# Kernel optimization log

Hardware: AMD Instinct MI355X
Metric: run time of the kernel (lower is better)

## Reference

```python
import jax, jax.numpy as jnp
import numpy as np

LMAX, MMAX = 4, 2
C_SPH = 32           # sphere_channels
H = 128              # edge hidden channels
N_SPECIES = 90
RESCALE = 5.0
M_SIZE_0 = LMAX + 1                                   # 5
NUM_COEFFS = sum(2 * min(l, MMAX) + 1 for l in range(LMAX + 1))  # 19
K_FULL = (LMAX + 1) ** 2                              # 25
N_NODES = 20000
N_EDGES = 320000
D_EDGE = 128
EPS = 1e-6


def layer_norm(x, scale, bias):
    mu = jnp.mean(x, axis=-1, keepdims=True)
    var = jnp.mean(jnp.square(x - mu), axis=-1, keepdims=True)
    return (x - mu) * jax.lax.rsqrt(var + EPS) * scale + bias


def setup_inputs() -> dict:
    key = jax.random.key(0)
    ks = jax.random.split(key, 12)
    node_species = jax.random.randint(ks[0], (N_NODES,), 0, N_SPECIES)
    edge_embeds = jax.random.normal(ks[1], (N_EDGES, D_EDGE), dtype=jnp.float32)
    senders = jax.random.randint(ks[2], (N_EDGES,), 0, N_NODES)
    receivers = jax.random.randint(ks[3], (N_EDGES,), 0, N_NODES)
    wigner_inv = jax.random.normal(ks[4], (N_EDGES, K_FULL, NUM_COEFFS), dtype=jnp.float32)
    # learned params
    embed_table = jax.random.normal(ks[5], (N_SPECIES, 2 * H), dtype=jnp.float32) * 0.001
    d_in = D_EDGE + 2 * H  # concat(edge, sender_emb, receiver_emb)
    W0 = jax.random.normal(ks[6], (d_in, H), dtype=jnp.float32) / np.sqrt(d_in)
    b0 = jnp.zeros((H,), jnp.float32)
    ln0_s = jnp.ones((H,), jnp.float32); ln0_b = jnp.zeros((H,), jnp.float32)
    W1 = jax.random.normal(ks[7], (H, H), dtype=jnp.float32) / np.sqrt(H)
    b1 = jnp.zeros((H,), jnp.float32)
    ln1_s = jnp.ones((H,), jnp.float32); ln1_b = jnp.zeros((H,), jnp.float32)
    W2 = jax.random.normal(ks[8], (H, M_SIZE_0 * C_SPH), dtype=jnp.float32) / np.sqrt(H)
    b2 = jnp.zeros((M_SIZE_0 * C_SPH,), jnp.float32)
    return dict(node_species=node_species, edge_embeds=edge_embeds, senders=senders,
                receivers=receivers, wigner_inv=wigner_inv, embed_table=embed_table,
                W0=W0, b0=b0, ln0_s=ln0_s, ln0_b=ln0_b,
                W1=W1, b1=b1, ln1_s=ln1_s, ln1_b=ln1_b, W2=W2, b2=b2)


def reference(node_species, edge_embeds, senders, receivers, wigner_inv, embed_table,
              W0, b0, ln0_s, ln0_b, W1, b1, ln1_s, ln1_b, W2, b2):
    num_nodes = node_species.shape[0]
    # atom edge embedding: gather + split
    node_emb = embed_table[node_species]                       # [N, 2H]
    s_emb, r_emb = jnp.split(node_emb, 2, axis=-1)             # [N, H] each
    x = jnp.concatenate((edge_embeds, s_emb[senders], r_emb[receivers]), axis=-1)  # [E, D+2H]
    # MLP with layer norm + silu between layers
    x = jax.nn.silu(layer_norm(x @ W0 + b0, ln0_s, ln0_b))
    x = jax.nn.silu(layer_norm(x @ W1 + b1, ln1_s, ln1_b))
    x = x @ W2 + b2                                            # [E, m0*C]
    feats_m_0 = x.reshape(-1, M_SIZE_0, C_SPH)                 # [E, 5, C]
    pad = jnp.zeros((x.shape[0], NUM_COEFFS - M_SIZE_0, C_SPH), dtype=x.dtype)
    edge_feats = jnp.concatenate((feats_m_0, pad), axis=1)     # [E, 19, C]
    # inverse wigner rotation back to full SH basis: [E, 25, C]
    edge_feats = jnp.einsum('ekm,emc->ekc', wigner_inv, edge_feats)
    node_feats = jax.ops.segment_sum(edge_feats, receivers, num_segments=num_nodes)
    return node_feats / RESCALE
```

## Files before the change

kernel.cpp:

```cpp
#include <hip/hip_runtime.h>
#include <hip/hip_bf16.h>
#include <cstddef>


#define MB 64
#define MTHREADS 512
#define DIN 384
#define HDIM 128
#define NOUT 160
#define NKF 25
#define WIG_LD 19
#define WIG_ROW 475

#define WP1OFF 98304
#define WP2OFF 131072
#define WPBYTES 172032

#define XS_B   784
#define FS_B   528
#define HS_B   272
#define REG0   0
#define REG1   50176
#define METAS  67584
#define METAR  67840
#define LDSSZ  68096

typedef __attribute__((ext_vector_type(8))) short short8;
typedef __attribute__((ext_vector_type(4))) float f32x4;

struct BF4 { __hip_bfloat162 a, b; };

__device__ __forceinline__ unsigned short f2bf(float f)
{
    union { float f; unsigned u; } x; x.f = f;
    unsigned r = x.u + 0x7fffu + ((x.u >> 16) & 1u);
    return (unsigned short)(r >> 16);
}

__global__ void pre_kernel(const int* __restrict__ recv, int* __restrict__ cnt,
                           int n_edges, int hgrid,
                           const float* __restrict__ W0, const float* __restrict__ W1,
                           const float* __restrict__ W2, unsigned short* __restrict__ Wp)
{
    const int bid = blockIdx.x;
    if (bid < hgrid) {
        const int e = bid * 256 + threadIdx.x;
        if (e < n_edges) atomicAdd(&cnt[recv[e]], 1);
        return;
    }
    const int id = (bid - hgrid) * 256 + threadIdx.x;
    const float* W; int k, n, NT, N; size_t base;
    if (id < 49152)      { W = W0; k = id >> 7;  n = id & 127;  NT = 8;  N = 128; base = 0; }
    else if (id < 65536) { int r = id - 49152; W = W1; k = r >> 7; n = r & 127; NT = 8; N = 128; base = 49152; }
    else if (id < 86016) { int r = id - 65536; W = W2; k = r / 160; n = r - 160 * k; NT = 10; N = 160; base = 65536; }
    else return;
    const float w = W[(size_t)k * N + n];
    const int kt = k >> 5, kk = k & 31;
    const int l = ((kk >> 3) << 4) | (n & 15);
    const int i = kk & 7;
    const int nt = n >> 4;
    Wp[base + (size_t)(kt * NT + nt) * 512 + l * 8 + i] = f2bf(w);
}

template<int NT, int KT>
__device__ __forceinline__ void gemm_tiles4(const char* __restrict__ ldsA, int astride,
                                            const char* __restrict__ wp,
                                            int nt, int lane, f32x4 acc[4])
{
    const int lr = lane & 15, lk = lane >> 4;
    short8 bcur = *(const short8*)(wp + (size_t)nt * 1024 + lane * 16);
#pragma unroll
    for (int kt = 0; kt < KT; ++kt) {
        short8 bnxt = bcur;
        if (kt + 1 < KT)
            bnxt = *(const short8*)(wp + (size_t)((kt + 1) * NT + nt) * 1024 + lane * 16);
        short8 a[4];
#pragma unroll
        for (int mt = 0; mt < 4; ++mt)
            a[mt] = *(const short8*)(ldsA + (mt * 16 + lr) * astride + kt * 64 + lk * 16);
#pragma unroll
        for (int mt = 0; mt < 4; ++mt)
            acc[mt] = __builtin_amdgcn_mfma_f32_16x16x32_bf16(a[mt], bcur, acc[mt], 0, 0, 0);
        bcur = bnxt;
    }
}

__device__ __forceinline__ void dump_acc4(char* Hf, int nt, int lane, const f32x4 acc[4],
                                          const float bias)
{
    const int lr = lane & 15, lk = lane >> 4;
#pragma unroll
    for (int mt = 0; mt < 4; ++mt)
#pragma unroll
        for (int i = 0; i < 4; ++i)
            *(float*)(Hf + (mt * 16 + lk * 4 + i) * FS_B + (nt * 16 + lr) * 4) = acc[mt][i] + bias;
}

__device__ __forceinline__ void ln_silu_bf(const char* Hf, char* Hb,
                                           const float* __restrict__ s,
                                           const float* __restrict__ b, int t)
{
    const int j = t & 7;
    const int r = t >> 3;
    float v[16];
    float sum = 0.f, sq = 0.f;
#pragma unroll
    for (int q4 = 0; q4 < 4; ++q4) {
        const float4 x4 = *(const float4*)(Hf + r * FS_B + (j * 16 + q4 * 4) * 4);
        v[q4 * 4 + 0] = x4.x; v[q4 * 4 + 1] = x4.y;
        v[q4 * 4 + 2] = x4.z; v[q4 * 4 + 3] = x4.w;
    }
#pragma unroll
    for (int q = 0; q < 16; ++q) { sum += v[q]; sq = fmaf(v[q], v[q], sq); }
#pragma unroll
    for (int m = 1; m < 8; m <<= 1) {
        sum += __shfl_xor(sum, m, 64);
        sq  += __shfl_xor(sq,  m, 64);
    }
    const float mu = sum * (1.f / 128.f);
    const float var = sq * (1.f / 128.f) - mu * mu;
    const float rstd = rsqrtf(var + 1e-6f);
#pragma unroll
    for (int q = 0; q < 16; q += 2) {
        const int c0 = j * 16 + q;
        float y0 = (v[q] - mu) * rstd * s[c0] + b[c0];
        float y1 = (v[q + 1] - mu) * rstd * s[c0 + 1] + b[c0 + 1];
        y0 = y0 / (1.f + __expf(-y0));
        y1 = y1 / (1.f + __expf(-y1));
        *(__hip_bfloat162*)(Hb + r * HS_B + c0 * 2) =
            __float22bfloat162_rn(make_float2(y0, y1));
    }
}

__global__ __launch_bounds__(MTHREADS, 2)
void mlp_mfma(
    const int* __restrict__ species,
    const float* __restrict__ edge_embeds,
    const int* __restrict__ senders,
    const int* __restrict__ receivers,
    const float* __restrict__ embed_table,
    const char* __restrict__ Wp,
    const float* __restrict__ b0, const float* __restrict__ ln0s, const float* __restrict__ ln0b,
    const float* __restrict__ b1, const float* __restrict__ ln1s, const float* __restrict__ ln1b,
    const float* __restrict__ b2,
    __hip_bfloat16* __restrict__ F,
    int* __restrict__ cursor, int* __restrict__ elist, int sgrid,
    int n_edges)
{
    __shared__ alignas(16) char lds[LDSSZ];

    const int bid = blockIdx.x;
    const int t = threadIdx.x;

    if (bid < sgrid) {
        const int e = bid * MTHREADS + t;
        if (e < n_edges) {
            const int p = atomicAdd(&cursor[receivers[e]], 1);
            elist[p] = e;
        }
        return;
    }

    int* sS = (int*)(lds + METAS);
    int* rS = (int*)(lds + METAR);

    const int e0 = (bid - sgrid) * MB;
    const int w = t >> 6;
    const int lane = t & 63;
    const int lr = lane & 15, lk = lane >> 4;

    if (t < MB) {
        const int e = e0 + t;
        int s = 0, r = 0;
        if (e < n_edges) { s = senders[e]; r = receivers[e]; }
        sS[t] = species[s];
        rS[t] = species[r];
    }
    __syncthreads();

    {
        const int row = t >> 3;
        const int e = e0 + row;
        const bool ev = e < n_edges;
        const int ss = sS[row], rr = rS[row];
        char* xrow = lds + REG0 + row * XS_B;
        const int c0 = (t & 7) * 4;
#pragma unroll
        for (int jj = 0; jj < 12; ++jj) {
            const int col = c0 + 32 * jj;
            float4 v = make_float4(0.f, 0.f, 0.f, 0.f);
            if (ev) {
                if (jj < 4)
                    v = *(const float4*)(edge_embeds + (size_t)e * 128 + col);
                else if (jj < 8)
                    v = *(const float4*)(embed_table + (size_t)ss * 256 + (col - 128));
                else
                    v = *(const float4*)(embed_table + (size_t)rr * 256 + 128 + (col - 256));
            }
            BF4 pk;
            pk.a = __float22bfloat162_rn(make_float2(v.x, v.y));
            pk.b = __float22bfloat162_rn(make_float2(v.z, v.w));
            *(BF4*)(xrow + col * 2) = pk;
        }
    }
    __syncthreads();

    const char* wp0 = Wp;
    const char* wp1 = Wp + WP1OFF;
    const char* wp2 = Wp + WP2OFF;

    f32x4 acc[4];

#pragma unroll
    for (int mt = 0; mt < 4; ++mt) acc[mt] = (f32x4){0.f, 0.f, 0.f, 0.f};
    gemm_tiles4<8, 12>(lds + REG0, XS_B, wp0, w, lane, acc);
    __syncthreads();
    dump_acc4(lds + REG0, w, lane, acc, b0[w * 16 + lr]);
    __syncthreads();
    ln_silu_bf(lds + REG0, lds + REG1, ln0s, ln0b, t);
    __syncthreads();

#pragma unroll
    for (int mt = 0; mt < 4; ++mt) acc[mt] = (f32x4){0.f, 0.f, 0.f, 0.f};
    gemm_tiles4<8, 4>(lds + REG1, HS_B, wp1, w, lane, acc);
    dump_acc4(lds + REG0, w, lane, acc, b1[w * 16 + lr]);
    __syncthreads();
    ln_silu_bf(lds + REG0, lds + REG1, ln1s, ln1b, t);
    __syncthreads();

#pragma unroll
    for (int p = 0; p < 2; ++p) {
        const int nt = w + 8 * p;
        if (nt >= 10) break;
#pragma unroll
        for (int mt = 0; mt < 4; ++mt) acc[mt] = (f32x4){0.f, 0.f, 0.f, 0.f};
        gemm_tiles4<10, 4>(lds + REG1, HS_B, wp2, nt, lane, acc);
        const float bb = b2[nt * 16 + lr];
#pragma unroll
        for (int mt = 0; mt < 4; ++mt)
#pragma unroll
            for (int i = 0; i < 4; ++i) {
                const int e = e0 + mt * 16 + lk * 4 + i;
                if (e < n_edges) {
                    union { unsigned short u; __hip_bfloat16 h; } cv;
                    cv.u = f2bf((acc[mt][i] + bb) * 0.2f);
                    F[(size_t)e * NOUT + nt * 16 + lr] = cv.h;
                }
            }
    }
}

#define SCAN_T 1024
#define SCAN_CH 20
__global__ __launch_bounds__(SCAN_T)
void scan_kernel(const int* __restrict__ cnt, int* __restrict__ offsets,
                 int* __restrict__ cursor, int n_nodes)
{
    __shared__ int waveSum[SCAN_T / 64];
    const int t = threadIdx.x;
    const int base = t * SCAN_CH;
    int local[SCAN_CH];
    int s = 0;
#pragma unroll
    for (int j = 0; j < SCAN_CH; ++j) {
        const int v = (base + j < n_nodes) ? cnt[base + j] : 0;
        local[j] = s;
        s += v;
    }
    const int lane = t & 63;
    int incl = s;
#pragma unroll
    for (int d = 1; d < 64; d <<= 1) {
        const int u = __shfl_up(incl, d, 64);
        if (lane >= d) incl += u;
    }
    if (lane == 63) waveSum[t >> 6] = incl;
    __syncthreads();
    if (t < SCAN_T / 64) {
        const int v = waveSum[t];
        int incl2 = v;
#pragma unroll
        for (int d = 1; d < SCAN_T / 64; d <<= 1) {
            const int u = __shfl_up(incl2, d, 64);
            if (lane >= d) incl2 += u;
        }
        waveSum[t] = incl2 - v;
    }
    __syncthreads();
    const int threadExcl = waveSum[t >> 6] + (incl - s);
#pragma unroll
    for (int j = 0; j < SCAN_CH; ++j)
        if (base + j < n_nodes) {
            const int o = threadExcl + local[j];
            offsets[base + j] = o;
            cursor[base + j] = o;
        }
    if (t == SCAN_T - 1) offsets[n_nodes] = threadExcl + s;
}

__global__ __launch_bounds__(256)
void agg_kernel(const float* __restrict__ wigner, const __hip_bfloat16* __restrict__ F,
                const int* __restrict__ offsets, const int* __restrict__ elist,
                float* __restrict__ out)
{
    const int n = blockIdx.x;
    const int t = threadIdx.x;
    __shared__ float wigS[2][128];

    const int beg = offsets[n];
    const int end = offsets[n + 1];

    const int ch = t & 31;
    const int k0 = t >> 5;
    float a0 = 0.f, a1 = 0.f, a2 = 0.f, a3 = 0.f;

    float f[5];
    if (beg < end) {
        const int e = elist[beg];
        if (t < 125) wigS[0][t] = wigner[(size_t)e * WIG_ROW + (t / 5) * WIG_LD + (t % 5)];
        const __hip_bfloat16* Fp = F + (size_t)e * NOUT + ch;
#pragma unroll
        for (int m = 0; m < 5; ++m) f[m] = __bfloat162float(Fp[m * 32]);
    }

    int buf = 0;
    for (int i = beg; i < end; ++i) {
        __syncthreads();
        float fc[5];
#pragma unroll
        for (int m = 0; m < 5; ++m) fc[m] = f[m];
        if (i + 1 < end) {
            const int e = elist[i + 1];
            if (t < 125) wigS[buf ^ 1][t] = wigner[(size_t)e * WIG_ROW + (t / 5) * WIG_LD + (t % 5)];
            const __hip_bfloat16* Fp = F + (size_t)e * NOUT + ch;
#pragma unroll
            for (int m = 0; m < 5; ++m) f[m] = __bfloat162float(Fp[m * 32]);
        }
        const float* wp = &wigS[buf][0];
        { const float* wq = wp + k0 * 5;        a0 += wq[0]*fc[0] + wq[1]*fc[1] + wq[2]*fc[2] + wq[3]*fc[3] + wq[4]*fc[4]; }
        { const float* wq = wp + (k0 + 8) * 5;  a1 += wq[0]*fc[0] + wq[1]*fc[1] + wq[2]*fc[2] + wq[3]*fc[3] + wq[4]*fc[4]; }
        { const float* wq = wp + (k0 + 16) * 5; a2 += wq[0]*fc[0] + wq[1]*fc[1] + wq[2]*fc[2] + wq[3]*fc[3] + wq[4]*fc[4]; }
        if (t < 32) { const float* wq = wp + 120; a3 += wq[0]*fc[0] + wq[1]*fc[1] + wq[2]*fc[2] + wq[3]*fc[3] + wq[4]*fc[4]; }
        buf ^= 1;
    }

    float* orow = out + (size_t)n * (NKF * 32);
    orow[t] = a0;
    orow[t + 256] = a1;
    orow[t + 512] = a2;
    if (t < 32) orow[t + 768] = a3;
}

#define EB 32
__device__ __forceinline__ void ln_silu_f(float (*Bx)[HDIM], const float* __restrict__ s,
                                          const float* __restrict__ b, int t)
{
    const int r = t >> 3;
    const int j = t & 7;
    float v[16];
    float sum = 0.f, sq = 0.f;
#pragma unroll
    for (int q = 0; q < 16; ++q) { v[q] = Bx[r][j*16+q]; sum += v[q]; sq = fmaf(v[q], v[q], sq); }
#pragma unroll
    for (int m = 1; m < 8; m <<= 1) { sum += __shfl_xor(sum, m, 64); sq += __shfl_xor(sq, m, 64); }
    const float mu = sum * (1.f/HDIM);
    const float var = sq * (1.f/HDIM) - mu*mu;
    const float rstd = rsqrtf(var + 1e-6f);
#pragma unroll
    for (int q = 0; q < 16; ++q) {
        const int cc = j*16+q;
        const float y = (v[q]-mu)*rstd*s[cc]+b[cc];
        Bx[r][cc] = y / (1.f + __expf(-y));
    }
}

__global__ __launch_bounds__(256, 2)
void edge_fused_kernel(
    const int* __restrict__ species, const float* __restrict__ edge_embeds,
    const int* __restrict__ senders, const int* __restrict__ receivers,
    const float* __restrict__ wigner, const float* __restrict__ embed_table,
    const float* __restrict__ W0, const float* __restrict__ b0,
    const float* __restrict__ ln0s, const float* __restrict__ ln0b,
    const float* __restrict__ W1, const float* __restrict__ b1,
    const float* __restrict__ ln1s, const float* __restrict__ ln1b,
    const float* __restrict__ W2, const float* __restrict__ b2,
    float* __restrict__ out, int n_edges)
{
    __shared__ float A[EB][DIN];
    __shared__ float Bx[EB][HDIM];
    __shared__ int sSpec[EB], rSpec[EB], rNode[EB];
    const int t = threadIdx.x;
    const int e0 = blockIdx.x * EB;
    if (t < EB) {
        const int e = e0 + t;
        int s = 0, r = 0;
        if (e < n_edges) { s = senders[e]; r = receivers[e]; }
        sSpec[t] = species[s]; rSpec[t] = species[r]; rNode[t] = r;
    }
    __syncthreads();
    for (int idx = t; idx < EB * DIN; idx += 256) {
        const int r = idx / DIN;
        const int i = idx - r * DIN;
        const int e = e0 + r;
        float v = 0.f;
        if (e < n_edges) {
            if (i < HDIM) v = edge_embeds[(size_t)e * HDIM + i];
            else if (i < 2*HDIM) v = embed_table[(size_t)sSpec[r]*256 + (i-HDIM)];
            else v = embed_table[(size_t)rSpec[r]*256 + HDIM + (i-2*HDIM)];
        }
        A[r][i] = v;
    }
    __syncthreads();
    const int c = t & (HDIM-1);
    const int g = t >> 7;
    float acc[16];
#pragma unroll
    for (int q = 0; q < 16; ++q) acc[q] = 0.f;
    for (int it = 0; it < DIN/4; ++it) {
        const float wa = W0[(4*it+0)*HDIM+c], wb = W0[(4*it+1)*HDIM+c];
        const float wc = W0[(4*it+2)*HDIM+c], wd = W0[(4*it+3)*HDIM+c];
#pragma unroll
        for (int q = 0; q < 16; ++q) {
            const float4 x4 = *reinterpret_cast<const float4*>(&A[g*16+q][4*it]);
            acc[q] = fmaf(x4.x, wa, fmaf(x4.y, wb, fmaf(x4.z, wc, fmaf(x4.w, wd, acc[q]))));
        }
    }
    { const float bb = b0[c];
#pragma unroll
      for (int q = 0; q < 16; ++q) Bx[g*16+q][c] = acc[q] + bb; }
    __syncthreads(); ln_silu_f(Bx, ln0s, ln0b, t); __syncthreads();
#pragma unroll
    for (int q = 0; q < 16; ++q) acc[q] = 0.f;
    for (int it = 0; it < HDIM/4; ++it) {
        const float wa = W1[(4*it+0)*HDIM+c], wb = W1[(4*it+1)*HDIM+c];
        const float wc = W1[(4*it+2)*HDIM+c], wd = W1[(4*it+3)*HDIM+c];
#pragma unroll
        for (int q = 0; q < 16; ++q) {
            const float4 x4 = *reinterpret_cast<const float4*>(&Bx[g*16+q][4*it]);
            acc[q] = fmaf(x4.x, wa, fmaf(x4.y, wb, fmaf(x4.z, wc, fmaf(x4.w, wd, acc[q]))));
        }
    }
    __syncthreads();
    { const float bb = b1[c];
#pragma unroll
      for (int q = 0; q < 16; ++q) Bx[g*16+q][c] = acc[q] + bb; }
    __syncthreads(); ln_silu_f(Bx, ln1s, ln1b, t); __syncthreads();
    float* Ff = &A[0][0];
    {
        float a2[16];
#pragma unroll
        for (int q = 0; q < 16; ++q) a2[q] = 0.f;
        for (int it = 0; it < HDIM/4; ++it) {
            const float wa = W2[(4*it+0)*NOUT+c], wb = W2[(4*it+1)*NOUT+c];
            const float wc = W2[(4*it+2)*NOUT+c], wd = W2[(4*it+3)*NOUT+c];
#pragma unroll
            for (int q = 0; q < 16; ++q) {
                const float4 x4 = *reinterpret_cast<const float4*>(&Bx[g*16+q][4*it]);
                a2[q] = fmaf(x4.x, wa, fmaf(x4.y, wb, fmaf(x4.z, wc, fmaf(x4.w, wd, a2[q]))));
            }
        }
        const float bb = b2[c];
#pragma unroll
        for (int q = 0; q < 16; ++q) Ff[(g*16+q)*NOUT+c] = (a2[q]+bb)*0.2f;
    }
    {
        const int c2 = HDIM + (t & 31);
        const int g8 = t >> 5;
        float a2[4] = {0.f, 0.f, 0.f, 0.f};
        for (int it = 0; it < HDIM/4; ++it) {
            const float wa = W2[(4*it+0)*NOUT+c2], wb = W2[(4*it+1)*NOUT+c2];
            const float wc = W2[(4*it+2)*NOUT+c2], wd = W2[(4*it+3)*NOUT+c2];
#pragma unroll
            for (int q = 0; q < 4; ++q) {
                const float4 x4 = *reinterpret_cast<const float4*>(&Bx[g8*4+q][4*it]);
                a2[q] = fmaf(x4.x, wa, fmaf(x4.y, wb, fmaf(x4.z, wc, fmaf(x4.w, wd, a2[q]))));
            }
        }
        const float bb = b2[c2];
#pragma unroll
        for (int q = 0; q < 4; ++q) Ff[(g8*4+q)*NOUT+c2] = (a2[q]+bb)*0.2f;
    }
    __syncthreads();
    for (int r = 0; r < EB; ++r) {
        const int e = e0 + r;
        if (e >= n_edges) break;
        const float* wrow = wigner + (size_t)e * WIG_ROW;
        float* orow = out + (size_t)rNode[r] * (NKF*32);
        const float* Fr = Ff + r * NOUT;
#pragma unroll
        for (int jj = 0; jj < 4; ++jj) {
            const int p = t + 256*jj;
            if (p < NKF*32) {
                const int k = p >> 5, chh = p & 31;
                float val = 0.f;
#pragma unroll
                for (int m = 0; m < 5; ++m)
                    val = fmaf(wrow[k*WIG_LD+m], Fr[m*32+chh], val);
                atomicAdd(&orow[p], val);
            }
        }
    }
}

extern "C" void kernel_launch(void* const* d_in, const int* in_sizes, int n_in,
                              void* d_out, int out_size, void* d_ws, size_t ws_size,
                              hipStream_t stream)
{
    const int*   species     = (const int*)d_in[0];
    const float* edge_embeds = (const float*)d_in[1];
    const int*   senders     = (const int*)d_in[2];
    const int*   receivers   = (const int*)d_in[3];
    const float* wigner      = (const float*)d_in[4];
    const float* embed_table = (const float*)d_in[5];
    const float* W0 = (const float*)d_in[6];
    const float* b0 = (const float*)d_in[7];
    const float* ln0s = (const float*)d_in[8];
    const float* ln0b = (const float*)d_in[9];
    const float* W1 = (const float*)d_in[10];
    const float* b1 = (const float*)d_in[11];
    const float* ln1s = (const float*)d_in[12];
    const float* ln1b = (const float*)d_in[13];
    const float* W2 = (const float*)d_in[14];
    const float* b2 = (const float*)d_in[15];
    float* out = (float*)d_out;

    const int n_nodes = in_sizes[0];
    const int n_edges = in_sizes[2];

    const size_t wpBytes   = WPBYTES;
    const size_t fBytes    = (size_t)n_edges * NOUT * sizeof(unsigned short);
    const size_t offBytes  = (size_t)(n_nodes + 1) * sizeof(int);
    const size_t curBytes  = (size_t)n_nodes * sizeof(int);
    const size_t listBytes = (size_t)n_edges * sizeof(int);
    const size_t need = wpBytes + fBytes + offBytes + curBytes + listBytes + 64;

    if (ws_size < need || n_nodes > SCAN_T * SCAN_CH || n_edges <= 0) {
        hipMemsetAsync(out, 0, (size_t)out_size * sizeof(float), stream);
        const int nblocks = (n_edges + EB - 1) / EB;
        hipLaunchKernelGGL(edge_fused_kernel, dim3(nblocks), dim3(256), 0, stream,
                           species, edge_embeds, senders, receivers, wigner, embed_table,
                           W0, b0, ln0s, ln0b, W1, b1, ln1s, ln1b, W2, b2, out, n_edges);
        return;
    }

    char* ws = (char*)d_ws;
    unsigned short* Wp = (unsigned short*)ws;
    __hip_bfloat16* F  = (__hip_bfloat16*)(ws + wpBytes);
    int*   offsets = (int*)(ws + wpBytes + fBytes);
    int*   cursor  = (int*)(ws + wpBytes + fBytes + offBytes);
    int*   elist   = (int*)(ws + wpBytes + fBytes + offBytes + curBytes);

    const int hgrid = (n_edges + 255) / 256;

    hipMemsetAsync(cursor, 0, curBytes, stream);
    hipLaunchKernelGGL(pre_kernel, dim3(hgrid + 336), dim3(256), 0, stream,
                       receivers, cursor, n_edges, hgrid, W0, W1, W2, Wp);

    hipLaunchKernelGGL(scan_kernel, dim3(1), dim3(SCAN_T), 0, stream,
                       cursor, offsets, cursor, n_nodes);

    const int sgrid = (n_edges + MTHREADS - 1) / MTHREADS;
    const int mblocks = (n_edges + MB - 1) / MB;
    hipLaunchKernelGGL(mlp_mfma, dim3(sgrid + mblocks), dim3(MTHREADS), 0, stream,
                       species, edge_embeds, senders, receivers, embed_table,
                       (const char*)Wp, b0, ln0s, ln0b, b1, ln1s, ln1b, b2,
                       F, cursor, elist, sgrid, n_edges);

    hipLaunchKernelGGL(agg_kernel, dim3(n_nodes), dim3(256), 0, stream,
                       wigner, F, offsets, elist, out);
}
```

Before: 479.5 us.

## Split first-layer input into double-buffered K-chunks overlapping gathers with MFMA

```diff
diff --git a/kernel.cpp b/kernel.cpp
--- a/kernel.cpp
+++ b/kernel.cpp
@@ -16,14 +16,15 @@
 #define WP2OFF 131072
 #define WPBYTES 172032
 
-#define XS_B   784
+#define XC_B   272
 #define FS_B   528
 #define HS_B   272
-#define REG0   0
-#define REG1   50176
-#define METAS  67584
-#define METAR  67840
-#define LDSSZ  68096
+#define XD0    0
+#define XD1    17408
+#define HBOFF  34816
+#define METAS  52224
+#define METAR  52480
+#define LDSSZ  52736
 
 typedef __attribute__((ext_vector_type(8))) short short8;
 typedef __attribute__((ext_vector_type(4))) float f32x4;
@@ -132,7 +133,7 @@
     }
 }
 
-__global__ __launch_bounds__(MTHREADS, 2)
+__global__ __launch_bounds__(MTHREADS, 6)
 void mlp_mfma(
     const int* __restrict__ species,
     const float* __restrict__ edge_embeds,
@@ -176,56 +177,77 @@
         sS[t] = species[s];
         rS[t] = species[r];
     }
-    __syncthreads();
+
+    const int srow = t >> 3;
+    const int se = e0 + srow;
+    const bool sev = se < n_edges;
+    const int sc0 = (t & 7) * 4;
+    char* xrow0 = lds + XD0 + srow * XC_B;
+    char* xrow1 = lds + XD1 + srow * XC_B;
+
+#pragma unroll
+    for (int jj = 0; jj < 4; ++jj) {
+        const int col = sc0 + 32 * jj;
+        float4 v = make_float4(0.f, 0.f, 0.f, 0.f);
+        if (sev) v = *(const float4*)(edge_embeds + (size_t)se * 128 + col);
+        BF4 pk;
+        pk.a = __float22bfloat162_rn(make_float2(v.x, v.y));
+        pk.b = __float22bfloat162_rn(make_float2(v.z, v.w));
+        *(BF4*)(xrow0 + col * 2) = pk;
+    }
+    __syncthreads();
+
+    const char* wp0 = Wp;
+    const char* wp1 = Wp + WP1OFF;
+    const char* wp2 = Wp + WP2OFF;
+
+    f32x4 acc[4];
+#pragma unroll
+    for (int mt = 0; mt < 4; ++mt) acc[mt] = (f32x4){0.f, 0.f, 0.f, 0.f};
 
     {
-        const int row = t >> 3;
-        const int e = e0 + row;
-        const bool ev = e < n_edges;
-        const int ss = sS[row], rr = rS[row];
-        char* xrow = lds + REG0 + row * XS_B;
-        const int c0 = (t & 7) * 4;
-#pragma unroll
-        for (int jj = 0; jj < 12; ++jj) {
-            const int col = c0 + 32 * jj;
+        const int ss = sS[srow], rr = rS[srow];
+#pragma unroll
+        for (int jj = 0; jj < 4; ++jj) {
+            const int col = sc0 + 32 * jj;
             float4 v = make_float4(0.f, 0.f, 0.f, 0.f);
-            if (ev) {
-                if (jj < 4)
-                    v = *(const float4*)(edge_embeds + (size_t)e * 128 + col);
-                else if (jj < 8)
-                    v = *(const float4*)(embed_table + (size_t)ss * 256 + (col - 128));
-                else
-                    v = *(const float4*)(embed_table + (size_t)rr * 256 + 128 + (col - 256));
-            }
+            if (sev) v = *(const float4*)(embed_table + (size_t)ss * 256 + col);
             BF4 pk;
             pk.a = __float22bfloat162_rn(make_float2(v.x, v.y));
             pk.b = __float22bfloat162_rn(make_float2(v.z, v.w));
-            *(BF4*)(xrow + col * 2) = pk;
-        }
-    }
-    __syncthreads();
-
-    const char* wp0 = Wp;
-    const char* wp1 = Wp + WP1OFF;
-    const char* wp2 = Wp + WP2OFF;
-
-    f32x4 acc[4];
+            *(BF4*)(xrow1 + col * 2) = pk;
+        }
+        gemm_tiles4<8, 4>(lds + XD0, XC_B, wp0, w, lane, acc);
+        __syncthreads();
+
+#pragma unroll
+        for (int jj = 0; jj < 4; ++jj) {
+            const int col = sc0 + 32 * jj;
+            float4 v = make_float4(0.f, 0.f, 0.f, 0.f);
+            if (sev) v = *(const float4*)(embed_table + (size_t)rr * 256 + 128 + col);
+            BF4 pk;
+            pk.a = __float22bfloat162_rn(make_float2(v.x, v.y));
+            pk.b = __float22bfloat162_rn(make_float2(v.z, v.w));
+            *(BF4*)(xrow0 + col * 2) = pk;
+        }
+        gemm_tiles4<8, 4>(lds + XD1, XC_B, wp0 + 4 * 8 * 1024, w, lane, acc);
+        __syncthreads();
+
+        gemm_tiles4<8, 4>(lds + XD0, XC_B, wp0 + 8 * 8 * 1024, w, lane, acc);
+        __syncthreads();
+    }
+
+    dump_acc4(lds + 0, w, lane, acc, b0[w * 16 + lr]);
+    __syncthreads();
+    ln_silu_bf(lds + 0, lds + HBOFF, ln0s, ln0b, t);
+    __syncthreads();
 
 #pragma unroll
     for (int mt = 0; mt < 4; ++mt) acc[mt] = (f32x4){0.f, 0.f, 0.f, 0.f};
-    gemm_tiles4<8, 12>(lds + REG0, XS_B, wp0, w, lane, acc);
-    __syncthreads();
-    dump_acc4(lds + REG0, w, lane, acc, b0[w * 16 + lr]);
-    __syncthreads();
-    ln_silu_bf(lds + REG0, lds + REG1, ln0s, ln0b, t);
-    __syncthreads();
-
-#pragma unroll
-    for (int mt = 0; mt < 4; ++mt) acc[mt] = (f32x4){0.f, 0.f, 0.f, 0.f};
-    gemm_tiles4<8, 4>(lds + REG1, HS_B, wp1, w, lane, acc);
-    dump_acc4(lds + REG0, w, lane, acc, b1[w * 16 + lr]);
-    __syncthreads();
-    ln_silu_bf(lds + REG0, lds + REG1, ln1s, ln1b, t);
+    gemm_tiles4<8, 4>(lds + HBOFF, HS_B, wp1, w, lane, acc);
+    dump_acc4(lds + 0, w, lane, acc, b1[w * 16 + lr]);
+    __syncthreads();
+    ln_silu_bf(lds + 0, lds + HBOFF, ln1s, ln1b, t);
     __syncthreads();
 
 #pragma unroll
@@ -234,7 +256,7 @@
         if (nt >= 10) break;
 #pragma unroll
         for (int mt = 0; mt < 4; ++mt) acc[mt] = (f32x4){0.f, 0.f, 0.f, 0.f};
-        gemm_tiles4<10, 4>(lds + REG1, HS_B, wp2, nt, lane, acc);
+        gemm_tiles4<10, 4>(lds + HBOFF, HS_B, wp2, nt, lane, acc);
         const float bb = b2[nt * 16 + lr];
 #pragma unroll
         for (int mt = 0; mt < 4; ++mt)
```

After: 526.2 us. 1.1x slower.
